# Kernel optimization log

Hardware: AMD Instinct MI355X
Metric: run time of the kernel (lower is better)

## Reference

```python
import jax, jax.numpy as jnp
import numpy as np

B, T, C, H = 4, 4096, 1024, 64

def setup_inputs() -> dict:
    key = jax.random.key(0)
    kx, kq, kk, kv = jax.random.split(key, 4)
    x = jax.random.normal(kx, (B, T, C), dtype=jnp.float32)
    Wq = jax.random.normal(kq, (C, H), dtype=jnp.float32) * (C ** -0.5)
    Wk = jax.random.normal(kk, (C, H), dtype=jnp.float32) * (C ** -0.5)
    Wv = jax.random.normal(kv, (C, H), dtype=jnp.float32) * (C ** -0.5)
    return {"x": x, "Wq": Wq, "Wk": Wk, "Wv": Wv}

def reference(x, Wq, Wk, Wv):
    # single-head causal attention, dropout p=0 (eval)
    q = jnp.einsum('btc,ch->bth', x, Wq)  # [B,T,H]
    k = jnp.einsum('btc,ch->bth', x, Wk)
    v = jnp.einsum('btc,ch->bth', x, Wv)
    scale = k.shape[-1] ** -0.5
    scores = jnp.einsum('bth,bsh->bts', q, k) * scale  # [B,T,T]
    causal = jnp.tril(jnp.ones((q.shape[1], q.shape[1]), dtype=bool))
    scores = jnp.where(causal, scores, -jnp.inf)
    weights = jax.nn.softmax(scores, axis=-1)
    out = jnp.einsum('bts,bsh->bth', weights, v)  # [B,T,H]
    return out
```

## Files before the change

### kernel.cpp

```cpp
#include <hip/hip_runtime.h>


typedef short  s16x8 __attribute__((ext_vector_type(8)));
typedef float  f32x4 __attribute__((ext_vector_type(4)));
typedef unsigned u32x2 __attribute__((ext_vector_type(2)));

constexpr int B = 4, T = 4096, C = 1024, H = 64;
constexpr int M = B * T;
constexpr float LOG2E = 1.44269504088896340736f;
constexpr float QSCALE = 0.125f * LOG2E;
constexpr float MBASE  = 4.0f * LOG2E;

__device__ __forceinline__ unsigned short f2bf(float f) {
    union { float f; unsigned u; } v; v.f = f;
    unsigned r = v.u + 0x7fffu + ((v.u >> 16) & 1u);
    return (unsigned short)(r >> 16);
}

__device__ __forceinline__ unsigned cvt_pk_bf16(float lo, float hi) {
    unsigned r;
    asm("v_cvt_pk_bf16_f32 %0, %1, %2" : "=v"(r) : "v"(lo), "v"(hi));
    return r;
}

__device__ __forceinline__ void gl_lds16(const void* g, void* l) {
    __builtin_amdgcn_global_load_lds(
        (const __attribute__((address_space(1))) unsigned*)g,
        (__attribute__((address_space(3))) unsigned*)l, 16, 0, 0);
}

__global__ void prep_w(const float* __restrict__ Wq, const float* __restrict__ Wk,
                       const float* __restrict__ Wv, unsigned short* __restrict__ Wt) {
    const int n = blockIdx.x;
    const float* W = (n < 64) ? Wq : (n < 128 ? Wk : Wv);
    const int col = n & 63;
    for (int k = threadIdx.x; k < C; k += blockDim.x)
        Wt[(size_t)n * C + k] = f2bf(W[(size_t)k * H + col]);
}

__global__ __launch_bounds__(512) void qkv_proj(
    const float* __restrict__ x, const unsigned short* __restrict__ Wt,
    unsigned short* __restrict__ Q, unsigned short* __restrict__ K,
    unsigned short* __restrict__ VT) {
    __shared__ __align__(16) unsigned short ldsA[2][32 * 64];
    __shared__ __align__(16) unsigned short ldsB[2][192 * 64];

    const int t = threadIdx.x, lane = t & 63, w = t >> 6;
    const int i = lane & 15, g = lane >> 4;
    const int rowbase = blockIdx.x * 32;
    const int rw = w & 1, nw = w >> 1;

    const int arow = t >> 3, aslot = t & 7;
    const float* aga = x + (size_t)(rowbase + arow) * C + ((aslot ^ (arow & 7)) * 8);
    const int awoff = arow * 64 + aslot * 8;
    const bool astage = (t < 256);

    const int brow8 = lane >> 3, bslot = lane & 7;
    const unsigned short* bga[3];
    int bn0[3];
#pragma unroll
    for (int j = 0; j < 3; ++j) {
        bn0[j] = w * 24 + j * 8;
        bga[j] = Wt + (size_t)(bn0[j] + brow8) * C + ((bslot ^ brow8) * 8);
    }

    f32x4 acc[3];
#pragma unroll
    for (int n = 0; n < 3; ++n) acc[n] = (f32x4){0.f, 0.f, 0.f, 0.f};

    {
#pragma unroll
        for (int j = 0; j < 3; ++j)
            gl_lds16(bga[j], &ldsB[0][bn0[j] * 64]);
        if (astage) {
            f32x4 a0 = *(const f32x4*)(aga);
            f32x4 a1 = *(const f32x4*)(aga + 4);
            union { unsigned u[4]; s16x8 v; } av;
            av.u[0] = cvt_pk_bf16(a0[0], a0[1]);
            av.u[1] = cvt_pk_bf16(a0[2], a0[3]);
            av.u[2] = cvt_pk_bf16(a1[0], a1[1]);
            av.u[3] = cvt_pk_bf16(a1[2], a1[3]);
            *(s16x8*)&ldsA[0][awoff] = av.v;
        }
    }
    __syncthreads();

    for (int it = 0; it < 16; ++it) {
        const int cur = it & 1, nxt = cur ^ 1;
        const int kc = (it + 1) * 64;
        f32x4 a0, a1;
        const bool more = (it < 15);
        if (more) {
            if (astage) {
                a0 = *(const f32x4*)(aga + kc);
                a1 = *(const f32x4*)(aga + kc + 4);
            }
#pragma unroll
            for (int j = 0; j < 3; ++j)
                gl_lds16(bga[j] + kc, &ldsB[nxt][bn0[j] * 64]);
        }
#pragma unroll
        for (int kst = 0; kst < 2; ++kst) {
            const int c = kst * 4 + g;
            s16x8 a = *(const s16x8*)&ldsA[cur][(rw * 16 + i) * 64 + ((c ^ (i & 7)) * 8)];
#pragma unroll
            for (int nt = 0; nt < 3; ++nt) {
                int n = nw * 48 + nt * 16 + i;
                s16x8 b = *(const s16x8*)&ldsB[cur][n * 64 + ((c ^ (i & 7)) * 8)];
                acc[nt] = __builtin_amdgcn_mfma_f32_16x16x32_bf16(a, b, acc[nt], 0, 0, 0);
            }
        }
        if (more && astage) {
            union { unsigned u[4]; s16x8 v; } av;
            av.u[0] = cvt_pk_bf16(a0[0], a0[1]);
            av.u[1] = cvt_pk_bf16(a0[2], a0[3]);
            av.u[2] = cvt_pk_bf16(a1[0], a1[1]);
            av.u[3] = cvt_pk_bf16(a1[2], a1[3]);
            *(s16x8*)&ldsA[nxt][awoff] = av.v;
        }
        __syncthreads();
    }

#pragma unroll
    for (int nt = 0; nt < 3; ++nt) {
        const int base = nw * 48 + nt * 16;
        const int n = base + i;
        if (base >= 128) {
            const int h = n - 128;
            const int bb = rowbase >> 12, tb = rowbase & 4095;
            u32x2 pk;
            pk[0] = cvt_pk_bf16(acc[nt][0], acc[nt][1]);
            pk[1] = cvt_pk_bf16(acc[nt][2], acc[nt][3]);
            *(u32x2*)(VT + (size_t)(bb * H + h) * T + tb + g * 8 + rw * 4) = pk;
        } else if (base >= 64) {
#pragma unroll
            for (int r = 0; r < 4; ++r)
                K[(size_t)(rowbase + rw * 16 + g * 4 + r) * H + (n - 64)] = f2bf(acc[nt][r]);
        } else {
#pragma unroll
            for (int r = 0; r < 4; ++r)
                Q[(size_t)(rowbase + rw * 16 + g * 4 + r) * H + n] = f2bf(acc[nt][r] * QSCALE);
        }
    }
}

__global__ __launch_bounds__(256) void attn(
    const unsigned short* __restrict__ Qg, const unsigned short* __restrict__ Kg,
    const unsigned short* __restrict__ VTg,
    unsigned short* __restrict__ Opb, float* __restrict__ lpart) {
    __shared__ __align__(16) unsigned short ks[2][64 * 64];
    __shared__ __align__(16) unsigned short vs[2][64 * 64];

    const int t = threadIdx.x, lane = t & 63, w = t >> 6;
    const int bid = blockIdx.x;
    const int b = bid & 3;
    const int sp = (bid >> 2) & 7;
    const int qt = 31 - (bid >> 5);
    const int q0 = qt * 128;
    const int q0w = q0 + w * 32;
    const int i = lane & 15, g = lane >> 4, g4 = g * 4;
    const int nkv = 2 * qt + 2;

    const unsigned short* Kb = Kg  + (size_t)b * T * H;
    const unsigned short* Vb = VTg + (size_t)b * H * T;

    const int r8 = lane >> 3, sl = lane & 7, sx = sl ^ r8;

    const unsigned short* QrowA = Qg + (size_t)(b * T + q0w + i) * H;
    s16x8 bqa0 = *(const s16x8*)(QrowA + g * 8);
    s16x8 bqa1 = *(const s16x8*)(QrowA + 32 + g * 8);
    const unsigned short* QrowB = QrowA + 16 * H;
    s16x8 bqb0 = *(const s16x8*)(QrowB + g * 8);
    s16x8 bqb1 = *(const s16x8*)(QrowB + 32 + g * 8);

    f32x4 oa[4], ob[4];
#pragma unroll
    for (int nt = 0; nt < 4; ++nt) {
        oa[nt] = (f32x4){0.f, 0.f, 0.f, 0.f};
        ob[nt] = (f32x4){0.f, 0.f, 0.f, 0.f};
    }
    float la = 0.f, lb = 0.f;

    if (sp < nkv) {
        const int kv0 = sp * 64;
#pragma unroll
        for (int j = 0; j < 2; ++j) {
            const int row = (w + j * 4) * 8 + r8;
            gl_lds16(Kb + (size_t)(kv0 + row) * H + sx * 8, &ks[0][row * 64 + sl * 8]);
            gl_lds16(Vb + (size_t)row * T + kv0 + sx * 8,   &vs[0][row * 64 + sl * 8]);
        }
    }
    __syncthreads();

    int cur = 0;
    for (int tile = sp; tile < nkv; tile += 8) {
        const int kv = tile * 64;
        if (tile + 8 < nkv) {
            const int kvn = kv + 512;
#pragma unroll
            for (int j = 0; j < 2; ++j) {
                const int row = (w + j * 4) * 8 + r8;
                gl_lds16(Kb + (size_t)(kvn + row) * H + sx * 8, &ks[cur ^ 1][row * 64 + sl * 8]);
                gl_lds16(Vb + (size_t)row * T + kvn + sx * 8,   &vs[cur ^ 1][row * 64 + sl * 8]);
            }
        }

        if (kv <= q0w + 31) {
            s16x8 kb[8];
#pragma unroll
            for (int kst = 0; kst < 2; ++kst)
#pragma unroll
                for (int nt = 0; nt < 4; ++nt)
                    kb[kst * 4 + nt] = *(const s16x8*)
                        &ks[cur][(nt * 16 + i) * 64 + (((kst * 4 + g) ^ (i & 7)) * 8)];

            unsigned pa[8], pb2[8];

            {
                f32x4 s[4];
#pragma unroll
                for (int nt = 0; nt < 4; ++nt)
                    s[nt] = (f32x4){-MBASE, -MBASE, -MBASE, -MBASE};
#pragma unroll
                for (int nt = 0; nt < 4; ++nt)
                    s[nt] = __builtin_amdgcn_mfma_f32_16x16x32_bf16(kb[nt], bqa0, s[nt], 0, 0, 0);
#pragma unroll
                for (int nt = 0; nt < 4; ++nt)
                    s[nt] = __builtin_amdgcn_mfma_f32_16x16x32_bf16(kb[4 + nt], bqa1, s[nt], 0, 0, 0);
                if (kv + 63 > q0w) {
                    const int thr = q0w + i - kv;
#pragma unroll
                    for (int nt = 0; nt < 4; ++nt)
#pragma unroll
                        for (int r = 0; r < 4; ++r)
                            if (nt * 16 + g4 + r > thr) s[nt][r] = -INFINITY;
                }
#pragma unroll
                for (int nt = 0; nt < 4; ++nt)
#pragma unroll
                    for (int r = 0; r < 4; ++r)
                        s[nt][r] = exp2f(s[nt][r]);
#pragma unroll
                for (int nt = 0; nt < 4; ++nt) {
                    pa[nt * 2]     = cvt_pk_bf16(s[nt][0], s[nt][1]);
                    pa[nt * 2 + 1] = cvt_pk_bf16(s[nt][2], s[nt][3]);
                }
                la += ((s[0][0] + s[0][1]) + (s[0][2] + s[0][3]))
                    + ((s[1][0] + s[1][1]) + (s[1][2] + s[1][3]))
                    + ((s[2][0] + s[2][1]) + (s[2][2] + s[2][3]))
                    + ((s[3][0] + s[3][1]) + (s[3][2] + s[3][3]));
            }

            {
                f32x4 s[4];
#pragma unroll
                for (int nt = 0; nt < 4; ++nt)
                    s[nt] = (f32x4){-MBASE, -MBASE, -MBASE, -MBASE};
#pragma unroll
                for (int nt = 0; nt < 4; ++nt)
                    s[nt] = __builtin_amdgcn_mfma_f32_16x16x32_bf16(kb[nt], bqb0, s[nt], 0, 0, 0);
#pragma unroll
                for (int nt = 0; nt < 4; ++nt)
                    s[nt] = __builtin_amdgcn_mfma_f32_16x16x32_bf16(kb[4 + nt], bqb1, s[nt], 0, 0, 0);
                if (kv + 63 > q0w + 16) {
                    const int thr = q0w + 16 + i - kv;
#pragma unroll
                    for (int nt = 0; nt < 4; ++nt)
#pragma unroll
                        for (int r = 0; r < 4; ++r)
                            if (nt * 16 + g4 + r > thr) s[nt][r] = -INFINITY;
                }
#pragma unroll
                for (int nt = 0; nt < 4; ++nt)
#pragma unroll
                    for (int r = 0; r < 4; ++r)
                        s[nt][r] = exp2f(s[nt][r]);
#pragma unroll
                for (int nt = 0; nt < 4; ++nt) {
                    pb2[nt * 2]     = cvt_pk_bf16(s[nt][0], s[nt][1]);
                    pb2[nt * 2 + 1] = cvt_pk_bf16(s[nt][2], s[nt][3]);
                }
                lb += ((s[0][0] + s[0][1]) + (s[0][2] + s[0][3]))
                    + ((s[1][0] + s[1][1]) + (s[1][2] + s[1][3]))
                    + ((s[2][0] + s[2][1]) + (s[2][2] + s[2][3]))
                    + ((s[3][0] + s[3][1]) + (s[3][2] + s[3][3]));
            }

            s16x8 vb[8];
#pragma unroll
            for (int kst = 0; kst < 2; ++kst)
#pragma unroll
                for (int nt = 0; nt < 4; ++nt)
                    vb[kst * 4 + nt] = *(const s16x8*)
                        &vs[cur][(nt * 16 + i) * 64 + (((kst * 4 + g) ^ (i & 7)) * 8)];

#pragma unroll
            for (int kst = 0; kst < 2; ++kst) {
                union { unsigned u[4]; s16x8 v; } fa, fb;
                fa.u[0] = pa[4 * kst];      fa.u[1] = pa[4 * kst + 1];
                fa.u[2] = pa[4 * kst + 2];  fa.u[3] = pa[4 * kst + 3];
                fb.u[0] = pb2[4 * kst];     fb.u[1] = pb2[4 * kst + 1];
                fb.u[2] = pb2[4 * kst + 2]; fb.u[3] = pb2[4 * kst + 3];
#pragma unroll
                for (int nt = 0; nt < 4; ++nt) {
                    oa[nt] = __builtin_amdgcn_mfma_f32_16x16x32_bf16(vb[kst * 4 + nt], fa.v, oa[nt], 0, 0, 0);
                    ob[nt] = __builtin_amdgcn_mfma_f32_16x16x32_bf16(vb[kst * 4 + nt], fb.v, ob[nt], 0, 0, 0);
                }
            }
        }

        __syncthreads();
        cur ^= 1;
    }

    la += __shfl_xor(la, 16);  la += __shfl_xor(la, 32);
    lb += __shfl_xor(lb, 16);  lb += __shfl_xor(lb, 32);
    unsigned short* opA = Opb + ((size_t)bid * 128 + w * 32 + i) * 64;
    unsigned short* opB = opA + 16 * 64;
#pragma unroll
    for (int nt = 0; nt < 4; ++nt) {
        u32x2 pk;
        pk[0] = cvt_pk_bf16(oa[nt][0], oa[nt][1]);
        pk[1] = cvt_pk_bf16(oa[nt][2], oa[nt][3]);
        *(u32x2*)(opA + nt * 16 + g4) = pk;
        pk[0] = cvt_pk_bf16(ob[nt][0], ob[nt][1]);
        pk[1] = cvt_pk_bf16(ob[nt][2], ob[nt][3]);
        *(u32x2*)(opB + nt * 16 + g4) = pk;
    }
    if (g == 0) {
        lpart[(size_t)bid * 128 + w * 32 + i]      = la;
        lpart[(size_t)bid * 128 + w * 32 + 16 + i] = lb;
    }
}

__global__ __launch_bounds__(256) void merge8(
    const unsigned short* __restrict__ Opb, const float* __restrict__ lpart,
    float* __restrict__ out) {
    const int idx = blockIdx.x * 256 + threadIdx.x;
    const int row = idx >> 4, c4 = (idx & 15) * 4;
    const int b = row >> 12, q = row & 4095;
    const int qt = q >> 7, r = q & 127;
    const int qti = 31 - qt;

    float L = 0.f;
    f32x4 o = (f32x4){0.f, 0.f, 0.f, 0.f};
#pragma unroll
    for (int sp = 0; sp < 8; ++sp) {
        const int bidp = qti * 32 + sp * 4 + b;
        L += lpart[(size_t)bidp * 128 + r];
        union { unsigned long long d; unsigned short s[4]; } v;
        v.d = *(const unsigned long long*)&Opb[((size_t)bidp * 128 + r) * 64 + c4];
#pragma unroll
        for (int k = 0; k < 4; ++k) {
            union { unsigned u; float f; } cv;
            cv.u = (unsigned)v.s[k] << 16;
            o[k] += cv.f;
        }
    }
    const float inv = 1.0f / L;
    f32x4 res = (f32x4){o[0] * inv, o[1] * inv, o[2] * inv, o[3] * inv};
    *(f32x4*)&out[(size_t)row * 64 + c4] = res;
}

extern "C" void kernel_launch(void* const* d_in, const int* in_sizes, int n_in,
                              void* d_out, int out_size, void* d_ws, size_t ws_size,
                              hipStream_t stream) {
    (void)in_sizes; (void)n_in; (void)out_size; (void)ws_size;
    const float* x  = (const float*)d_in[0];
    const float* Wq = (const float*)d_in[1];
    const float* Wk = (const float*)d_in[2];
    const float* Wv = (const float*)d_in[3];
    float* out = (float*)d_out;

    char* ws = (char*)d_ws;
    unsigned short* Q  = (unsigned short*)(ws);
    unsigned short* K  = (unsigned short*)(ws + (size_t)1 * M * H * 2);
    unsigned short* VT = (unsigned short*)(ws + (size_t)3 * M * H * 2);
    unsigned short* Wt = (unsigned short*)(ws + (size_t)4 * M * H * 2);
    unsigned short* Opb = (unsigned short*)(ws + (size_t)4 * M * H * 2 + 512 * 1024);
    float* lpart = (float*)(ws + (size_t)4 * M * H * 2 + 512 * 1024
                            + (size_t)1024 * 128 * 64 * 2);

    prep_w<<<192, 256, 0, stream>>>(Wq, Wk, Wv, Wt);
    qkv_proj<<<M / 32, 512, 0, stream>>>(x, Wt, Q, K, VT);
    attn<<<1024, 256, 0, stream>>>(Q, K, VT, Opb, lpart);
    merge8<<<1024, 256, 0, stream>>>(Opb, lpart, out);
}
```

Before: 56.03 us.

## Fuse split-KV merge into attention kernel via last-block atomic counter

```diff
diff --git a/kernel.cpp b/kernel.cpp
--- a/kernel.cpp
+++ b/kernel.cpp
@@ -147,15 +147,18 @@
 __global__ __launch_bounds__(256) void attn(
     const unsigned short* __restrict__ Qg, const unsigned short* __restrict__ Kg,
     const unsigned short* __restrict__ VTg,
-    unsigned short* __restrict__ Opb, float* __restrict__ lpart) {
+    unsigned short* __restrict__ Opb, float* __restrict__ lpart,
+    int* __restrict__ sem, float* __restrict__ out) {
     __shared__ __align__(16) unsigned short ks[2][64 * 64];
     __shared__ __align__(16) unsigned short vs[2][64 * 64];
+    __shared__ int lastFlag;
 
     const int t = threadIdx.x, lane = t & 63, w = t >> 6;
     const int bid = blockIdx.x;
     const int b = bid & 3;
     const int sp = (bid >> 2) & 7;
-    const int qt = 31 - (bid >> 5);
+    const int qti = bid >> 5;
+    const int qt = 31 - qti;
     const int q0 = qt * 128;
     const int q0w = q0 + w * 32;
     const int i = lane & 15, g = lane >> 4, g4 = g * 4;
@@ -331,35 +334,40 @@
         lpart[(size_t)bid * 128 + w * 32 + i]      = la;
         lpart[(size_t)bid * 128 + w * 32 + 16 + i] = lb;
     }
-}
-
-__global__ __launch_bounds__(256) void merge8(
-    const unsigned short* __restrict__ Opb, const float* __restrict__ lpart,
-    float* __restrict__ out) {
-    const int idx = blockIdx.x * 256 + threadIdx.x;
-    const int row = idx >> 4, c4 = (idx & 15) * 4;
-    const int b = row >> 12, q = row & 4095;
-    const int qt = q >> 7, r = q & 127;
-    const int qti = 31 - qt;
-
-    float L = 0.f;
-    f32x4 o = (f32x4){0.f, 0.f, 0.f, 0.f};
-#pragma unroll
-    for (int sp = 0; sp < 8; ++sp) {
-        const int bidp = qti * 32 + sp * 4 + b;
-        L += lpart[(size_t)bidp * 128 + r];
-        union { unsigned long long d; unsigned short s[4]; } v;
-        v.d = *(const unsigned long long*)&Opb[((size_t)bidp * 128 + r) * 64 + c4];
-#pragma unroll
-        for (int k = 0; k < 4; ++k) {
-            union { unsigned u; float f; } cv;
-            cv.u = (unsigned)v.s[k] << 16;
-            o[k] += cv.f;
-        }
-    }
-    const float inv = 1.0f / L;
-    f32x4 res = (f32x4){o[0] * inv, o[1] * inv, o[2] * inv, o[3] * inv};
-    *(f32x4*)&out[(size_t)row * 64 + c4] = res;
+
+    __threadfence();
+    __syncthreads();
+    if (t == 0) {
+        int prev = atomicAdd(&sem[qti * 4 + b], 1);
+        lastFlag = (prev == 7) ? 1 : 0;
+    }
+    __syncthreads();
+    if (lastFlag == 0) return;
+    __threadfence();
+
+    for (int item = t; item < 2048; item += 256) {
+        const int r = item >> 4, c4 = (item & 15) * 4;
+        float L = 0.f;
+        f32x4 o = (f32x4){0.f, 0.f, 0.f, 0.f};
+#pragma unroll
+        for (int sp2 = 0; sp2 < 8; ++sp2) {
+            const int bidp = qti * 32 + sp2 * 4 + b;
+            L += __hip_atomic_load(&lpart[(size_t)bidp * 128 + r],
+                                   __ATOMIC_RELAXED, __HIP_MEMORY_SCOPE_AGENT);
+            unsigned long long d = __hip_atomic_load(
+                (const unsigned long long*)&Opb[((size_t)bidp * 128 + r) * 64 + c4],
+                __ATOMIC_RELAXED, __HIP_MEMORY_SCOPE_AGENT);
+#pragma unroll
+            for (int k = 0; k < 4; ++k) {
+                union { unsigned u; float f; } cv;
+                cv.u = (unsigned)((d >> (16 * k)) & 0xFFFFu) << 16;
+                o[k] += cv.f;
+            }
+        }
+        const float inv = 1.0f / L;
+        f32x4 res = (f32x4){o[0] * inv, o[1] * inv, o[2] * inv, o[3] * inv};
+        *(f32x4*)&out[((size_t)(b * T + q0 + r)) * 64 + c4] = res;
+    }
 }
 
 extern "C" void kernel_launch(void* const* d_in, const int* in_sizes, int n_in,
@@ -380,9 +388,11 @@
     unsigned short* Opb = (unsigned short*)(ws + (size_t)4 * M * H * 2 + 512 * 1024);
     float* lpart = (float*)(ws + (size_t)4 * M * H * 2 + 512 * 1024
                             + (size_t)1024 * 128 * 64 * 2);
-
+    int* sem = (int*)(ws + (size_t)4 * M * H * 2 + 512 * 1024
+                      + (size_t)1024 * 128 * 64 * 2 + 1024 * 1024);
+
+    hipMemsetAsync(sem, 0, 128 * sizeof(int), stream);
     prep_w<<<192, 256, 0, stream>>>(Wq, Wk, Wv, Wt);
     qkv_proj<<<M / 32, 512, 0, stream>>>(x, Wt, Q, K, VT);
-    attn<<<1024, 256, 0, stream>>>(Q, K, VT, Opb, lpart);
-    merge8<<<1024, 256, 0, stream>>>(Opb, lpart, out);
-}
+    attn<<<1024, 256, 0, stream>>>(Q, K, VT, Opb, lpart, sem, out);
+}
```

New measurement: 209.7 us. +274.2%, slower.

## Triple-buffer K/V tiles with prefetch distance two and partial vmcnt waits

Applied to the files above, without the earlier changes.

```diff
diff --git a/kernel.cpp b/kernel.cpp
--- a/kernel.cpp
+++ b/kernel.cpp
@@ -148,8 +148,8 @@
     const unsigned short* __restrict__ Qg, const unsigned short* __restrict__ Kg,
     const unsigned short* __restrict__ VTg,
     unsigned short* __restrict__ Opb, float* __restrict__ lpart) {
-    __shared__ __align__(16) unsigned short ks[2][64 * 64];
-    __shared__ __align__(16) unsigned short vs[2][64 * 64];
+    __shared__ __align__(16) unsigned short ks[3][64 * 64];
+    __shared__ __align__(16) unsigned short vs[3][64 * 64];
 
     const int t = threadIdx.x, lane = t & 63, w = t >> 6;
     const int bid = blockIdx.x;
@@ -160,6 +160,7 @@
     const int q0w = q0 + w * 32;
     const int i = lane & 15, g = lane >> 4, g4 = g * 4;
     const int nkv = 2 * qt + 2;
+    const int nTiles = (sp < nkv) ? ((nkv - sp + 7) >> 3) : 0;
 
     const unsigned short* Kb = Kg  + (size_t)b * T * H;
     const unsigned short* Vb = VTg + (size_t)b * H * T;
@@ -181,7 +182,7 @@
     }
     float la = 0.f, lb = 0.f;
 
-    if (sp < nkv) {
+    if (nTiles > 0) {
         const int kv0 = sp * 64;
 #pragma unroll
         for (int j = 0; j < 2; ++j) {
@@ -190,18 +191,33 @@
             gl_lds16(Vb + (size_t)row * T + kv0 + sx * 8,   &vs[0][row * 64 + sl * 8]);
         }
     }
-    __syncthreads();
-
-    int cur = 0;
-    for (int tile = sp; tile < nkv; tile += 8) {
+    if (nTiles > 1) {
+        const int kv1 = (sp + 8) * 64;
+#pragma unroll
+        for (int j = 0; j < 2; ++j) {
+            const int row = (w + j * 4) * 8 + r8;
+            gl_lds16(Kb + (size_t)(kv1 + row) * H + sx * 8, &ks[1][row * 64 + sl * 8]);
+            gl_lds16(Vb + (size_t)row * T + kv1 + sx * 8,   &vs[1][row * 64 + sl * 8]);
+        }
+        asm volatile("s_waitcnt vmcnt(4)\n\ts_barrier" ::: "memory");
+    } else {
+        asm volatile("s_waitcnt vmcnt(0)\n\ts_barrier" ::: "memory");
+    }
+
+    for (int n = 0; n < nTiles; ++n) {
+        const int tile = sp + n * 8;
         const int kv = tile * 64;
-        if (tile + 8 < nkv) {
-            const int kvn = kv + 512;
+        const int cur = n % 3;
+        const bool issue = (n + 2 < nTiles);
+
+        if (issue) {
+            const int nxt = (n + 2) % 3;
+            const int kvn = kv + 1024;
 #pragma unroll
             for (int j = 0; j < 2; ++j) {
                 const int row = (w + j * 4) * 8 + r8;
-                gl_lds16(Kb + (size_t)(kvn + row) * H + sx * 8, &ks[cur ^ 1][row * 64 + sl * 8]);
-                gl_lds16(Vb + (size_t)row * T + kvn + sx * 8,   &vs[cur ^ 1][row * 64 + sl * 8]);
+                gl_lds16(Kb + (size_t)(kvn + row) * H + sx * 8, &ks[nxt][row * 64 + sl * 8]);
+                gl_lds16(Vb + (size_t)row * T + kvn + sx * 8,   &vs[nxt][row * 64 + sl * 8]);
             }
         }
 
@@ -309,8 +325,8 @@
             }
         }
 
-        __syncthreads();
-        cur ^= 1;
+        if (issue) asm volatile("s_waitcnt vmcnt(4)\n\ts_barrier" ::: "memory");
+        else       asm volatile("s_waitcnt vmcnt(0)\n\ts_barrier" ::: "memory");
     }
 
     la += __shfl_xor(la, 16);  la += __shfl_xor(la, 32);
```

New measurement: 53.65 us. 1.04x faster.
